# Kernel optimization log

Hardware: AMD Instinct MI355X
Metric: run time of the kernel (lower is better)

## Reference

```python
import jax, jax.numpy as jnp
import numpy as np

B, CELL, K, T, V = 4096, 400, 10, 256, 80

def setup_inputs() -> dict:
    key = jax.random.key(0)
    k1, k2, k3, k4 = jax.random.split(key, 4)
    x = jax.random.normal(k1, (B, CELL), dtype=jnp.float32)
    kappa_old = jax.random.uniform(k2, (B, K), dtype=jnp.float32)
    onehots = jax.random.uniform(k3, (B, T, V), dtype=jnp.float32)
    # Linear(cell_size, 3*K): weight [3K, CELL], bias [3K]; scale like torch default
    W = jax.random.normal(k4, (3 * K, CELL), dtype=jnp.float32) / jnp.sqrt(CELL).astype(jnp.float32)
    b = jnp.zeros((3 * K,), dtype=jnp.float32)
    return {"x": x, "kappa_old": kappa_old, "onehots": onehots, "W": W, "b": b, "text_len": T}

def reference(x, kappa_old, onehots, W, b, text_len):
    params = x @ W.T + b                       # [B, 3K]
    alpha = jnp.exp(params[:, :K])             # [B, K]
    beta = jnp.exp(params[:, K:2 * K])         # [B, K]
    kappa = kappa_old + jnp.exp(params[:, 2 * K:])  # [B, K]
    u = jnp.arange(text_len, dtype=x.dtype)    # [T]
    # gravity = -beta * (kappa - u)^2, broadcast over text positions
    gravity = -beta[:, :, None] * (kappa[:, :, None] - u) ** 2   # [B, K, T]
    phi = jnp.sum(alpha[:, :, None] * jnp.exp(gravity), axis=1)  # [B, T]
    weight = jnp.einsum('bt,btv->bv', phi, onehots)              # [B, V]
    return weight, kappa
```

## Files before the change

kernel.cpp:

```cpp
#include <hip/hip_runtime.h>

#define BB   4096
#define CELL 400
#define KK   10
#define TT   256
#define VV   80

__global__ __launch_bounds__(320) void window_kernel(
    const float* __restrict__ x,
    const float* __restrict__ kappa_old,
    const float* __restrict__ onehots,
    const float* __restrict__ W,
    const float* __restrict__ bias,
    float* __restrict__ out)
{
    __shared__ float  x_lds[CELL];
    __shared__ float  p_lds[30];
    __shared__ float  alpha_lds[KK], beta_lds[KK], kappa_lds[KK];
    __shared__ float  phi_lds[TT];
    __shared__ float4 part_lds[320];

    const int b   = blockIdx.x;
    const int tid = threadIdx.x;

    if (tid < 100) {
        const float4* x4 = (const float4*)(x + (size_t)b * CELL);
        ((float4*)x_lds)[tid] = x4[tid];
    }
    __syncthreads();

    if (tid < 240) {
        const int j = tid >> 3;
        const int r = tid & 7;
        const float* wrow = W + j * CELL + r * 50;
        const float* xs   = x_lds + r * 50;
        float s = 0.f;
        #pragma unroll
        for (int i = 0; i < 50; ++i) s += xs[i] * wrow[i];
        s += __shfl_down(s, 4, 8);
        s += __shfl_down(s, 2, 8);
        s += __shfl_down(s, 1, 8);
        if (r == 0) p_lds[j] = s + bias[j];
    }
    __syncthreads();

    if (tid < KK) {
        float a  = __expf(p_lds[tid]);
        float be = __expf(p_lds[KK + tid]);
        float ka = kappa_old[(size_t)b * KK + tid] + __expf(p_lds[2 * KK + tid]);
        alpha_lds[tid] = a;
        beta_lds[tid]  = be;
        kappa_lds[tid] = ka;
        out[(size_t)BB * VV + (size_t)b * KK + tid] = ka;
    }
    __syncthreads();

    if (tid < TT) {
        const float u = (float)tid;
        float s = 0.f;
        #pragma unroll
        for (int k = 0; k < KK; ++k) {
            float d = kappa_lds[k] - u;
            s += alpha_lds[k] * __expf(-beta_lds[k] * d * d);
        }
        phi_lds[tid] = s;
    }
    __syncthreads();

    {
        const float4* oh4 = (const float4*)(onehots + (size_t)b * TT * VV);
        const int g = tid / 20;
        float4 acc = {0.f, 0.f, 0.f, 0.f};
        #pragma unroll
        for (int it = 0; it < 16; ++it) {
            const int t = g + 16 * it;
            const float ph = phi_lds[t];
            const float4 o = oh4[tid + 320 * it];
            acc.x += ph * o.x;
            acc.y += ph * o.y;
            acc.z += ph * o.z;
            acc.w += ph * o.w;
        }
        part_lds[tid] = acc;
    }
    __syncthreads();

    if (tid < 20) {
        float4 s = {0.f, 0.f, 0.f, 0.f};
        #pragma unroll
        for (int g = 0; g < 16; ++g) {
            const float4 p = part_lds[g * 20 + tid];
            s.x += p.x; s.y += p.y; s.z += p.z; s.w += p.w;
        }
        float4* o4 = (float4*)(out + (size_t)b * VV);
        o4[tid] = s;
    }
}

extern "C" void kernel_launch(void* const* d_in, const int* in_sizes, int n_in,
                              void* d_out, int out_size, void* d_ws, size_t ws_size,
                              hipStream_t stream) {
    const float* x         = (const float*)d_in[0];
    const float* kappa_old = (const float*)d_in[1];
    const float* onehots   = (const float*)d_in[2];
    const float* W         = (const float*)d_in[3];
    const float* bias      = (const float*)d_in[4];
    float* out = (float*)d_out;

    window_kernel<<<BB, 320, 0, stream>>>(x, kappa_old, onehots, W, bias, out);
}
```

Measured before the change: 447.9 us.

## Split into wave-per-row phi kernel and separate onehot einsum kernel

Splits the fused kernel into two launches. The first computes the projection, alpha/beta/kappa and phi with one wavefront per batch row, using shuffle reductions and no LDS or block barriers, and writes phi to workspace. The second streams the onehots and reduces them against phi loaded from workspace. This removes the serial, barrier-heavy prologue from the bandwidth-bound einsum blocks, at the cost of an extra launch and a phi round-trip through global memory.

New measurement: 462.9 us. 3.3% more time.

```diff
diff --git a/kernel.cpp b/kernel.cpp
--- a/kernel.cpp
+++ b/kernel.cpp
@@ -6,94 +6,113 @@
 #define TT   256
 #define VV   80
 
-__global__ __launch_bounds__(320) void window_kernel(
+__global__ __launch_bounds__(256) void phi_kernel(
     const float* __restrict__ x,
     const float* __restrict__ kappa_old,
-    const float* __restrict__ onehots,
     const float* __restrict__ W,
     const float* __restrict__ bias,
+    float* __restrict__ out,
+    float* __restrict__ phi)
+{
+    const int tid  = threadIdx.x;
+    const int lane = tid & 63;
+    const int wav  = tid >> 6;
+    const int b    = blockIdx.x * 4 + wav;
+
+    float xr[7];
+    const float* xrow = x + (size_t)b * CELL;
+    #pragma unroll
+    for (int c = 0; c < 7; ++c) {
+        const int i = lane + 64 * c;
+        xr[c] = (i < CELL) ? xrow[i] : 0.f;
+    }
+
+    float acc0 = 0.f, acc1 = 0.f, acc2 = 0.f, acc3 = 0.f;
+
+    #pragma unroll
+    for (int k = 0; k < KK; ++k) {
+        float pa = 0.f, pb = 0.f, pc = 0.f;
+        const float* wa = W + (size_t)k * CELL;
+        const float* wb = W + (size_t)(k + KK) * CELL;
+        const float* wc = W + (size_t)(k + 2 * KK) * CELL;
+        #pragma unroll
+        for (int c = 0; c < 7; ++c) {
+            const int i = lane + 64 * c;
+            if (i < CELL) {
+                pa += xr[c] * wa[i];
+                pb += xr[c] * wb[i];
+                pc += xr[c] * wc[i];
+            }
+        }
+        #pragma unroll
+        for (int m = 32; m >= 1; m >>= 1) {
+            pa += __shfl_xor(pa, m, 64);
+            pb += __shfl_xor(pb, m, 64);
+            pc += __shfl_xor(pc, m, 64);
+        }
+        const float a  = __expf(pa + bias[k]);
+        const float be = __expf(pb + bias[k + KK]);
+        const float ka = kappa_old[(size_t)b * KK + k] + __expf(pc + bias[k + 2 * KK]);
+        if (lane == k) out[(size_t)BB * VV + (size_t)b * KK + k] = ka;
+
+        {
+            float d0 = ka - (float)(lane);
+            float d1 = ka - (float)(lane + 64);
+            float d2 = ka - (float)(lane + 128);
+            float d3 = ka - (float)(lane + 192);
+            acc0 += a * __expf(-be * d0 * d0);
+            acc1 += a * __expf(-be * d1 * d1);
+            acc2 += a * __expf(-be * d2 * d2);
+            acc3 += a * __expf(-be * d3 * d3);
+        }
+    }
+
+    float* ph = phi + (size_t)b * TT;
+    ph[lane]       = acc0;
+    ph[lane + 64]  = acc1;
+    ph[lane + 128] = acc2;
+    ph[lane + 192] = acc3;
+}
+
+__global__ __launch_bounds__(320) void einsum_kernel(
+    const float* __restrict__ onehots,
+    const float* __restrict__ phi,
     float* __restrict__ out)
 {
-    __shared__ float  x_lds[CELL];
-    __shared__ float  p_lds[30];
-    __shared__ float  alpha_lds[KK], beta_lds[KK], kappa_lds[KK];
     __shared__ float  phi_lds[TT];
     __shared__ float4 part_lds[320];
 
     const int b   = blockIdx.x;
     const int tid = threadIdx.x;
 
-    if (tid < 100) {
-        const float4* x4 = (const float4*)(x + (size_t)b * CELL);
-        ((float4*)x_lds)[tid] = x4[tid];
+    if (tid < 64) {
+        ((float4*)phi_lds)[tid] = ((const float4*)(phi + (size_t)b * TT))[tid];
     }
     __syncthreads();
 
-    if (tid < 240) {
-        const int j = tid >> 3;
-        const int r = tid & 7;
-        const float* wrow = W + j * CELL + r * 50;
-        const float* xs   = x_lds + r * 50;
-        float s = 0.f;
-        #pragma unroll
-        for (int i = 0; i < 50; ++i) s += xs[i] * wrow[i];
-        s += __shfl_down(s, 4, 8);
-        s += __shfl_down(s, 2, 8);
-        s += __shfl_down(s, 1, 8);
-        if (r == 0) p_lds[j] = s + bias[j];
+    const float4* oh4 = (const float4*)(onehots + (size_t)b * TT * VV);
+    const int g = tid / 20;
+    float4 acc = {0.f, 0.f, 0.f, 0.f};
+    #pragma unroll
+    for (int it = 0; it < 16; ++it) {
+        const float  ph = phi_lds[g + 16 * it];
+        const float4 o  = oh4[tid + 320 * it];
+        acc.x += ph * o.x;
+        acc.y += ph * o.y;
+        acc.z += ph * o.z;
+        acc.w += ph * o.w;
     }
-    __syncthreads();
-
-    if (tid < KK) {
-        float a  = __expf(p_lds[tid]);
-        float be = __expf(p_lds[KK + tid]);
-        float ka = kappa_old[(size_t)b * KK + tid] + __expf(p_lds[2 * KK + tid]);
-        alpha_lds[tid] = a;
-        beta_lds[tid]  = be;
-        kappa_lds[tid] = ka;
-        out[(size_t)BB * VV + (size_t)b * KK + tid] = ka;
-    }
-    __syncthreads();
-
-    if (tid < TT) {
-        const float u = (float)tid;
-        float s = 0.f;
-        #pragma unroll
-        for (int k = 0; k < KK; ++k) {
-            float d = kappa_lds[k] - u;
-            s += alpha_lds[k] * __expf(-beta_lds[k] * d * d);
-        }
-        phi_lds[tid] = s;
-    }
-    __syncthreads();
-
-    {
-        const float4* oh4 = (const float4*)(onehots + (size_t)b * TT * VV);
-        const int g = tid / 20;
-        float4 acc = {0.f, 0.f, 0.f, 0.f};
-        #pragma unroll
-        for (int it = 0; it < 16; ++it) {
-            const int t = g + 16 * it;
-            const float ph = phi_lds[t];
-            const float4 o = oh4[tid + 320 * it];
-            acc.x += ph * o.x;
-            acc.y += ph * o.y;
-            acc.z += ph * o.z;
-            acc.w += ph * o.w;
-        }
-        part_lds[tid] = acc;
-    }
+    part_lds[tid] = acc;
     __syncthreads();
 
     if (tid < 20) {
         float4 s = {0.f, 0.f, 0.f, 0.f};
         #pragma unroll
-        for (int g = 0; g < 16; ++g) {
-            const float4 p = part_lds[g * 20 + tid];
+        for (int gg = 0; gg < 16; ++gg) {
+            const float4 p = part_lds[gg * 20 + tid];
             s.x += p.x; s.y += p.y; s.z += p.z; s.w += p.w;
         }
-        float4* o4 = (float4*)(out + (size_t)b * VV);
-        o4[tid] = s;
+        ((float4*)(out + (size_t)b * VV))[tid] = s;
     }
 }
 
@@ -106,6 +125,8 @@
     const float* W         = (const float*)d_in[3];
     const float* bias      = (const float*)d_in[4];
     float* out = (float*)d_out;
+    float* phi = (float*)d_ws;
 
-    window_kernel<<<BB, 320, 0, stream>>>(x, kappa_old, onehots, W, bias, out);
+    phi_kernel<<<BB / 4, 256, 0, stream>>>(x, kappa_old, W, bias, out, phi);
+    einsum_kernel<<<BB, 320, 0, stream>>>(onehots, phi, out);
 }
```

## Prefetch onehots into registers up front and use wave-wide matvec reduction

Applied to the files above, without the earlier changes.

Each thread now issues all 16 float4 onehots loads at kernel start into registers, so the dominant memory stream overlaps with the matvec, exp and phi stages instead of starting after them. The matvec is restructured so each wave computes six output rows with x held in registers, reduced by a 64-lane xor shuffle. This drops the x staging in shared memory and one barrier. The cost is 64 extra VGPRs per thread for the prefetched data, which may reduce occupancy.

Result: slower. 459.0 us (+2.5%).

```diff
diff --git a/kernel.cpp b/kernel.cpp
--- a/kernel.cpp
+++ b/kernel.cpp
@@ -6,7 +6,7 @@
 #define TT   256
 #define VV   80
 
-__global__ __launch_bounds__(320) void window_kernel(
+__global__ __launch_bounds__(320) void window_fused(
     const float* __restrict__ x,
     const float* __restrict__ kappa_old,
     const float* __restrict__ onehots,
@@ -14,40 +14,51 @@
     const float* __restrict__ bias,
     float* __restrict__ out)
 {
-    __shared__ float  x_lds[CELL];
     __shared__ float  p_lds[30];
     __shared__ float  alpha_lds[KK], beta_lds[KK], kappa_lds[KK];
     __shared__ float  phi_lds[TT];
     __shared__ float4 part_lds[320];
 
-    const int b   = blockIdx.x;
-    const int tid = threadIdx.x;
+    const int b    = blockIdx.x;
+    const int tid  = threadIdx.x;
+    const int lane = tid & 63;
+    const int wav  = tid >> 6;
 
-    if (tid < 100) {
-        const float4* x4 = (const float4*)(x + (size_t)b * CELL);
-        ((float4*)x_lds)[tid] = x4[tid];
+    const float4* oh4 = (const float4*)(onehots + (size_t)b * TT * VV);
+    float4 o[16];
+    #pragma unroll
+    for (int it = 0; it < 16; ++it) o[it] = oh4[tid + 320 * it];
+
+    float ko = 0.f;
+    if (tid < KK) ko = kappa_old[(size_t)b * KK + tid];
+
+    float xr[7];
+    const float* xrow = x + (size_t)b * CELL;
+    #pragma unroll
+    for (int c = 0; c < 7; ++c) {
+        const int i = lane + 64 * c;
+        xr[c] = (i < CELL) ? xrow[i] : 0.f;
     }
-    __syncthreads();
-
-    if (tid < 240) {
-        const int j = tid >> 3;
-        const int r = tid & 7;
-        const float* wrow = W + j * CELL + r * 50;
-        const float* xs   = x_lds + r * 50;
+    #pragma unroll
+    for (int r = 0; r < 6; ++r) {
+        const int j = wav * 6 + r;
+        const float* wrow = W + (size_t)j * CELL;
         float s = 0.f;
         #pragma unroll
-        for (int i = 0; i < 50; ++i) s += xs[i] * wrow[i];
-        s += __shfl_down(s, 4, 8);
-        s += __shfl_down(s, 2, 8);
-        s += __shfl_down(s, 1, 8);
-        if (r == 0) p_lds[j] = s + bias[j];
+        for (int c = 0; c < 7; ++c) {
+            const int i = lane + 64 * c;
+            if (i < CELL) s += xr[c] * wrow[i];
+        }
+        #pragma unroll
+        for (int m = 32; m >= 1; m >>= 1) s += __shfl_xor(s, m, 64);
+        if (lane == 0) p_lds[j] = s + bias[j];
     }
     __syncthreads();
 
     if (tid < KK) {
-        float a  = __expf(p_lds[tid]);
-        float be = __expf(p_lds[KK + tid]);
-        float ka = kappa_old[(size_t)b * KK + tid] + __expf(p_lds[2 * KK + tid]);
+        const float a  = __expf(p_lds[tid]);
+        const float be = __expf(p_lds[KK + tid]);
+        const float ka = ko + __expf(p_lds[2 * KK + tid]);
         alpha_lds[tid] = a;
         beta_lds[tid]  = be;
         kappa_lds[tid] = ka;
@@ -60,7 +71,7 @@
         float s = 0.f;
         #pragma unroll
         for (int k = 0; k < KK; ++k) {
-            float d = kappa_lds[k] - u;
+            const float d = kappa_lds[k] - u;
             s += alpha_lds[k] * __expf(-beta_lds[k] * d * d);
         }
         phi_lds[tid] = s;
@@ -68,18 +79,15 @@
     __syncthreads();
 
     {
-        const float4* oh4 = (const float4*)(onehots + (size_t)b * TT * VV);
         const int g = tid / 20;
         float4 acc = {0.f, 0.f, 0.f, 0.f};
         #pragma unroll
         for (int it = 0; it < 16; ++it) {
-            const int t = g + 16 * it;
-            const float ph = phi_lds[t];
-            const float4 o = oh4[tid + 320 * it];
-            acc.x += ph * o.x;
-            acc.y += ph * o.y;
-            acc.z += ph * o.z;
-            acc.w += ph * o.w;
+            const float ph = phi_lds[g + 16 * it];
+            acc.x += ph * o[it].x;
+            acc.y += ph * o[it].y;
+            acc.z += ph * o[it].z;
+            acc.w += ph * o[it].w;
         }
         part_lds[tid] = acc;
     }
@@ -92,8 +100,7 @@
             const float4 p = part_lds[g * 20 + tid];
             s.x += p.x; s.y += p.y; s.z += p.z; s.w += p.w;
         }
-        float4* o4 = (float4*)(out + (size_t)b * VV);
-        o4[tid] = s;
+        ((float4*)(out + (size_t)b * VV))[tid] = s;
     }
 }
 
@@ -107,5 +114,5 @@
     const float* bias      = (const float*)d_in[4];
     float* out = (float*)d_out;
 
-    window_kernel<<<BB, 320, 0, stream>>>(x, kappa_old, onehots, W, bias, out);
+    window_fused<<<BB, 320, 0, stream>>>(x, kappa_old, onehots, W, bias, out);
 }
```
